# Optimization experiments

Hardware: AMD Instinct MI355X
Metric: run time of the kernel (lower is better)

The kernel has to match this reference:

```python
import jax, jax.numpy as jnp
import numpy as np

IN_F = 4096
OUT_F = 11008
GROUPSIZE = 128
N_GROUPS = IN_F // GROUPSIZE  # 32


def setup_inputs() -> dict:
    key = jax.random.key(0)
    k1, k2, k3, k4 = jax.random.split(key, 4)
    x = jax.random.normal(k1, (4, 2048, IN_F), dtype=jnp.float32)
    # packed 4-bit weights: 8 nibbles per int32 along the input dim
    qweight = jax.random.randint(k2, (IN_F // 8, OUT_F), 0, 2**31 - 1, dtype=jnp.int32)
    # packed 4-bit zero points: 8 nibbles per int32 along the output dim
    qzeros = jax.random.randint(k3, (N_GROUPS, OUT_F // 8), 0, 2**31 - 1, dtype=jnp.int32)
    scales = jax.random.uniform(k4, (N_GROUPS, OUT_F), dtype=jnp.float32,
                                minval=0.001, maxval=0.01)
    g_idx = (jnp.arange(IN_F, dtype=jnp.int32) // GROUPSIZE).astype(jnp.int32)
    return {"x": x, "qweight": qweight, "scales": scales,
            "qzeros": qzeros, "g_idx": g_idx}


def _dequantize(qweight, scales, qzeros, g_idx):
    """GPTQ v2 dequant: W[i, j] = scales[g_idx[i], j] * (q[i, j] - (z[g_idx[i], j] + 1))."""
    shifts = jnp.arange(8, dtype=jnp.int32) * 4  # nibble shift amounts
    # unpack weights along input dim: [in/8, 8, out] -> [in, out]
    q = (qweight[:, None, :] >> shifts[None, :, None]) & 0xF
    q = q.reshape(-1, qweight.shape[1]).astype(scales.dtype)
    # unpack zeros along output dim: [g, out/8, 8] -> [g, out]; +1 per GPTQ v2
    z = ((qzeros[:, :, None] >> shifts[None, None, :]) & 0xF) + 1
    z = z.reshape(qzeros.shape[0], -1).astype(scales.dtype)
    return scales[g_idx] * (q - z[g_idx])  # [in, out]


def reference(x, qweight, scales, qzeros, g_idx):
    W = _dequantize(qweight, scales, qzeros, g_idx)  # [IN_F, OUT_F]
    return jnp.einsum('bsi,io->bso', x, W)
```

## Files before the change

### kernel.cpp

```cpp
#include <hip/hip_runtime.h>
#include <hip/hip_bf16.h>

#define IN_F 4096
#define OUT_F 11008

typedef __bf16 bf16_t;
typedef bf16_t bf16x8 __attribute__((ext_vector_type(8)));
typedef float f32x4 __attribute__((ext_vector_type(4)));
typedef unsigned int u32;

__global__ __launch_bounds__(256) void cvt_x_kernel(const float* __restrict__ x,
                                                    bf16_t* __restrict__ xb) {
    size_t i = ((size_t)blockIdx.x * 256 + threadIdx.x) * 8;
    f32x4 v0 = __builtin_nontemporal_load((const f32x4*)(x + i));
    f32x4 v1 = __builtin_nontemporal_load((const f32x4*)(x + i + 4));
    bf16x8 h;
    h[0]=(bf16_t)v0[0]; h[1]=(bf16_t)v0[1]; h[2]=(bf16_t)v0[2]; h[3]=(bf16_t)v0[3];
    h[4]=(bf16_t)v1[0]; h[5]=(bf16_t)v1[1]; h[6]=(bf16_t)v1[2]; h[7]=(bf16_t)v1[3];
    *(bf16x8*)(xb + i) = h;
}


#define NI (IN_F / 128)

__global__ __launch_bounds__(512, 2) void gemm_dq(const bf16_t* __restrict__ A,
                                                  const int* __restrict__ qweight,
                                                  const float* __restrict__ scales,
                                                  const int* __restrict__ qzeros,
                                                  float* __restrict__ C) {
    __shared__ __align__(16) bf16_t smemA[2 * 2 * 128 * 64];

    const int tid  = threadIdx.x;
    const int lane = tid & 63;
    const int wid  = tid >> 6;
    const int wr   = wid >> 2;
    const int wc   = wid & 3;

    const int bid = blockIdx.x;
    const int swz = (bid & 7) * 172 + (bid >> 3);
    const int bx = swz % 43;
    const int by = swz / 43;
    const int m0 = by * 256;
    const int n0 = bx * 256;

    int lr0, kb0, lr1, kb1;
    {
        int L0 = tid * 16;
        int p0 = L0 ^ (((L0 >> 7) & 7) << 4);
        lr0 = p0 >> 7; kb0 = (p0 & 127) >> 1;
        int L1 = (512 + tid) * 16;
        int p1 = L1 ^ (((L1 >> 7) & 7) << 4);
        lr1 = p1 >> 7; kb1 = (p1 & 127) >> 1;
    }

    const int xm = (lane & 7) << 4;
    const int arow = lane & 15;
    int colk[2];
    #pragma unroll
    for (int ks = 0; ks < 2; ++ks)
        colk[ks] = ((ks * 64) + ((lane >> 4) * 16)) ^ xm;

    const int ncol = n0 + wc * 64 + (lane & 15);
    const int qidx = (lane >> 4) * OUT_F + ncol;
    const int zidx = ncol >> 3;
    const int zsh  = (lane & 7) * 4;

#define STAGE_A(buf, half, koff)                                                           \
    do {                                                                                   \
        const bf16_t* g0_ = A + (size_t)(m0 + (half) * 128 + lr0) * IN_F + (koff) + kb0;   \
        __builtin_amdgcn_global_load_lds(                                                  \
            (const __attribute__((address_space(1))) u32*)g0_,                             \
            (__attribute__((address_space(3))) u32*)((char*)smemA + (buf) * 32768 +        \
                                                     (half) * 16384 + wid * 1024),         \
            16, 0, 0);                                                                     \
        const bf16_t* g1_ = A + (size_t)(m0 + (half) * 128 + lr1) * IN_F + (koff) + kb1;   \
        __builtin_amdgcn_global_load_lds(                                                  \
            (const __attribute__((address_space(1))) u32*)g1_,                             \
            (__attribute__((address_space(3))) u32*)((char*)smemA + (buf) * 32768 +        \
                                                     (half) * 16384 + 8192 + wid * 1024),  \
            16, 0, 0);                                                                     \
    } while (0)

#define RD_A(dst, buf, mbase)                                                              \
    _Pragma("unroll") for (int mm = 0; mm < 4; ++mm)                                       \
    _Pragma("unroll") for (int ks = 0; ks < 2; ++ks)                                       \
        dst[mm * 2 + ks] = *(const bf16x8*)((const char*)smemA + (buf) * 32768 +           \
            wr * 16384 + (((mbase) + mm) * 16 + arow) * 128 + colk[ks]);

#define LOAD_W(rowAbs)                                                                     \
    _Pragma("unroll") for (int nt = 0; nt < 4; ++nt)                                       \
    _Pragma("unroll") for (int ks = 0; ks < 2; ++ks)                                       \
        w[nt * 2 + ks] = ((const u32*)qweight)[qidx + ((rowAbs) + ks * 4) * OUT_F + nt * 16];

#define DEQ(dst, nt0)                                                                      \
    _Pragma("unroll") for (int nn = 0; nn < 2; ++nn)                                       \
    _Pragma("unroll") for (int ks = 0; ks < 2; ++ks) {                                     \
        const u32 wv_ = w[((nt0) + nn) * 2 + ks];                                          \
        const u32 ev_ = wv_ & 0x0F0F0F0Fu;                                                 \
        const u32 od_ = (wv_ >> 4) & 0x0F0F0F0Fu;                                          \
        const float s_ = s0[(nt0) + nn];                                                   \
        const float z_ = nsz0[(nt0) + nn];                                                 \
        bf16x8 h_;                                                                         \
        h_[0] = (bf16_t)fmaf((float)(ev_ & 0xFF), s_, z_);                                 \
        h_[1] = (bf16_t)fmaf((float)(od_ & 0xFF), s_, z_);                                 \
        h_[2] = (bf16_t)fmaf((float)((ev_ >> 8) & 0xFF), s_, z_);                          \
        h_[3] = (bf16_t)fmaf((float)((od_ >> 8) & 0xFF), s_, z_);                          \
        h_[4] = (bf16_t)fmaf((float)((ev_ >> 16) & 0xFF), s_, z_);                         \
        h_[5] = (bf16_t)fmaf((float)((od_ >> 16) & 0xFF), s_, z_);                         \
        h_[6] = (bf16_t)fmaf((float)(ev_ >> 24), s_, z_);                                  \
        h_[7] = (bf16_t)fmaf((float)(od_ >> 24), s_, z_);                                  \
        dst[nn * 2 + ks] = h_;                                                             \
    }

#define MFMA_Q(aArr, bArr, mbase, nbase)                                                   \
    __builtin_amdgcn_s_setprio(1);                                                         \
    _Pragma("unroll") for (int mm = 0; mm < 4; ++mm)                                       \
    _Pragma("unroll") for (int nn = 0; nn < 2; ++nn)                                       \
    _Pragma("unroll") for (int ks = 0; ks < 2; ++ks)                                       \
        acc[(mbase) + mm][(nbase) + nn] = __builtin_amdgcn_mfma_f32_16x16x32_bf16(         \
            aArr[mm * 2 + ks], bArr[nn * 2 + ks], acc[(mbase) + mm][(nbase) + nn],         \
            0, 0, 0);                                                                      \
    __builtin_amdgcn_s_setprio(0);

#define SCHED0() __builtin_amdgcn_sched_barrier(0)
#define BAR() do { SCHED0(); __builtin_amdgcn_s_barrier(); } while (0)
#define VMCNT10() asm volatile("s_waitcnt vmcnt(10)" ::: "memory")
#define VMCNT8()  asm volatile("s_waitcnt vmcnt(8)"  ::: "memory")

    f32x4 acc[8][4];
    #pragma unroll
    for (int m = 0; m < 8; ++m)
        #pragma unroll
        for (int n = 0; n < 4; ++n)
            acc[m][n] = (f32x4)0.0f;

    bf16x8 aR[8], b01[4], b23[4];
    u32   w[8];
    float s0[4], nsz0[4];
    float sraw[4]; u32 zraw[4];

    STAGE_A(0, 0, 0); STAGE_A(0, 1, 0);
    STAGE_A(1, 0, 64);
    LOAD_W(0);
    #pragma unroll
    for (int nt = 0; nt < 4; ++nt) {
        sraw[nt] = scales[ncol + nt * 16];
        zraw[nt] = ((const u32*)qzeros)[zidx + nt * 2];
    }
    #pragma unroll
    for (int nt = 0; nt < 4; ++nt) {
        s0[nt] = sraw[nt];
        nsz0[nt] = -sraw[nt] * (float)(((zraw[nt] >> zsh) & 0xF) + 1);
    }
    BAR();

    for (int i = 0; i < NI; ++i) {
        const int  kc = i * 128;
        const int  kn = kc + 128;
        const int  rw = i * 16;
        const bool nl = (i + 1 < NI);

        RD_A(aR, 0, 0);
        STAGE_A(1, 1, kc + 64);
        DEQ(b01, 0);
        MFMA_Q(aR, b01, 0, 0);
        BAR();
        DEQ(b23, 2);
        MFMA_Q(aR, b23, 0, 2);
        BAR();
        RD_A(aR, 0, 4);
        LOAD_W(rw + 8);
        MFMA_Q(aR, b01, 4, 0);
        BAR();
        if (nl) STAGE_A(0, 0, kn);
        MFMA_Q(aR, b23, 4, 2);
        if (nl) VMCNT10(); else VMCNT8();
        BAR();
        RD_A(aR, 1, 0);
        if (nl) STAGE_A(0, 1, kn);
        DEQ(b01, 0);
        MFMA_Q(aR, b01, 0, 0);
        BAR();
        if (nl) {
            #pragma unroll
            for (int nt = 0; nt < 4; ++nt) {
                sraw[nt] = scales[ncol + (i + 1) * OUT_F + nt * 16];
                zraw[nt] = ((const u32*)qzeros)[zidx + (i + 1) * (OUT_F / 8) + nt * 2];
            }
        }
        DEQ(b23, 2);
        MFMA_Q(aR, b23, 0, 2);
        BAR();
        RD_A(aR, 1, 4);
        if (nl) {
            LOAD_W(rw + 16);
            #pragma unroll
            for (int nt = 0; nt < 4; ++nt) {
                s0[nt] = sraw[nt];
                nsz0[nt] = -sraw[nt] * (float)(((zraw[nt] >> zsh) & 0xF) + 1);
            }
        }
        MFMA_Q(aR, b01, 4, 0);
        BAR();
        if (nl) STAGE_A(1, 0, kn + 64);
        MFMA_Q(aR, b23, 4, 2);
        if (nl) VMCNT10();
        BAR();
    }

    const int cn  = lane & 15;
    const int cr4 = (lane >> 4) * 4;
    #pragma unroll
    for (int m = 0; m < 8; ++m) {
        #pragma unroll
        for (int r = 0; r < 4; ++r) {
            const int grow = m0 + wr * 128 + m * 16 + cr4 + r;
            float* orow = C + (size_t)grow * OUT_F + n0 + wc * 64 + cn;
            #pragma unroll
            for (int n = 0; n < 4; ++n)
                orow[n * 16] = acc[m][n][r];
        }
    }
}

#define BMf 128
#define BNf 128
#define BKf 32
#define LDPF 40

__global__ __launch_bounds__(256, 2) void gptq_gemm_fused(
    const float* __restrict__ x, const int* __restrict__ qweight,
    const float* __restrict__ scales, const int* __restrict__ qzeros,
    float* __restrict__ out)
{
    __shared__ bf16_t As[BMf * LDPF];
    __shared__ bf16_t Bs[BNf * LDPF];
    const int tid = threadIdx.x, lane = tid & 63, wid = tid >> 6;
    const int wr = wid >> 1, wc = wid & 1;
    const int m0 = blockIdx.y * BMf, n0 = blockIdx.x * BNf;
    const int a_row = tid >> 2, a_slot = tid & 3;
    const int b_k8l = tid >> 7, b_n = tid & 127;

    f32x4 acc[4][4];
    #pragma unroll
    for (int i = 0; i < 4; ++i)
        #pragma unroll
        for (int j = 0; j < 4; ++j) acc[i][j] = (f32x4)0.0f;

    for (int kt = 0; kt < IN_F / BKf; ++kt) {
        const int k0 = kt * BKf;
        const int g  = k0 >> 7;
        __syncthreads();
        #pragma unroll
        for (int p = 0; p < 2; ++p) {
            const int row = a_row + p * 64;
            const float* src = x + (size_t)(m0 + row) * IN_F + k0 + a_slot * 8;
            f32x4 v0 = *(const f32x4*)src;
            f32x4 v1 = *(const f32x4*)(src + 4);
            bf16x8 h;
            h[0]=(bf16_t)v0[0]; h[1]=(bf16_t)v0[1]; h[2]=(bf16_t)v0[2]; h[3]=(bf16_t)v0[3];
            h[4]=(bf16_t)v1[0]; h[5]=(bf16_t)v1[1]; h[6]=(bf16_t)v1[2]; h[7]=(bf16_t)v1[3];
            *(bf16x8*)(&As[row * LDPF + a_slot * 8]) = h;
        }
        {
            const int gn = n0 + b_n;
            const float s  = scales[(size_t)g * OUT_F + gn];
            const int   zw = qzeros[(size_t)g * (OUT_F / 8) + (gn >> 3)];
            const float sz = s * (float)(((zw >> ((gn & 7) * 4)) & 0xF) + 1);
            #pragma unroll
            for (int p = 0; p < 2; ++p) {
                const int k8l = b_k8l + p * 2;
                const int w = qweight[(size_t)(k0 / 8 + k8l) * OUT_F + gn];
                bf16x8 h;
                #pragma unroll
                for (int j = 0; j < 8; ++j)
                    h[j] = (bf16_t)fmaf((float)((w >> (4 * j)) & 0xF), s, -sz);
                *(bf16x8*)(&Bs[b_n * LDPF + k8l * 8]) = h;
            }
        }
        __syncthreads();
        bf16x8 af[4], bfr[4];
        #pragma unroll
        for (int m = 0; m < 4; ++m)
            af[m] = *(const bf16x8*)(&As[(wr * 64 + m * 16 + (lane & 15)) * LDPF + (lane >> 4) * 8]);
        #pragma unroll
        for (int n = 0; n < 4; ++n)
            bfr[n] = *(const bf16x8*)(&Bs[(wc * 64 + n * 16 + (lane & 15)) * LDPF + (lane >> 4) * 8]);
        #pragma unroll
        for (int m = 0; m < 4; ++m)
            #pragma unroll
            for (int n = 0; n < 4; ++n)
                acc[m][n] = __builtin_amdgcn_mfma_f32_16x16x32_bf16(af[m], bfr[n], acc[m][n], 0, 0, 0);
    }
    const int cn = lane & 15, cr4 = (lane >> 4) * 4;
    #pragma unroll
    for (int m = 0; m < 4; ++m)
        #pragma unroll
        for (int r = 0; r < 4; ++r) {
            const int grow = m0 + wr * 64 + m * 16 + cr4 + r;
            float* orow = out + (size_t)grow * OUT_F + n0 + wc * 64 + cn;
            #pragma unroll
            for (int n = 0; n < 4; ++n) orow[n * 16] = acc[m][n][r];
        }
}

extern "C" void kernel_launch(void* const* d_in, const int* in_sizes, int n_in,
                              void* d_out, int out_size, void* d_ws, size_t ws_size,
                              hipStream_t stream) {
    const float* x       = (const float*)d_in[0];
    const int*   qweight = (const int*)d_in[1];
    const float* scales  = (const float*)d_in[2];
    const int*   qzeros  = (const int*)d_in[3];
    float* out = (float*)d_out;

    const int M = in_sizes[0] / IN_F;
    const size_t xb_bytes = (size_t)M * IN_F * 2;

    if (ws_size >= xb_bytes && (M % 256) == 0) {
        bf16_t* xb = (bf16_t*)d_ws;
        cvt_x_kernel<<<dim3((M * IN_F) / (256 * 8)), dim3(256), 0, stream>>>(x, xb);
        const int nwg = (OUT_F / 256) * (M / 256);
        gemm_dq<<<dim3(nwg), dim3(512), 0, stream>>>(xb, qweight, scales, qzeros, out);
    } else {
        gptq_gemm_fused<<<dim3(OUT_F / BNf, M / BMf), dim3(256), 0, stream>>>(
            x, qweight, scales, qzeros, out);
    }
}
```

Measured before the change: 1.001 ms.

## Stage packed 4-bit weights through LDS with async global-to-LDS loads

Packed qweight tiles are now loaded cooperatively into a double-buffered shared-memory region with global_load_lds, instead of each wave issuing strided per-lane global loads into registers. Dequantization of a whole k-half is moved to a single point after the corresponding vmcnt wait, and the scale/zero loads are rescheduled earlier. The aim is coalesced 16-byte weight fetches that overlap the MFMA work. The cost is 16 KB of extra LDS, changed wait counts, and dequant bursts that are less interleaved with the MFMAs.

```diff
diff --git a/kernel.cpp b/kernel.cpp
--- a/kernel.cpp
+++ b/kernel.cpp
@@ -23,12 +23,13 @@
 
 #define NI (IN_F / 128)
 
-__global__ __launch_bounds__(512, 2) void gemm_dq(const bf16_t* __restrict__ A,
+__global__ __launch_bounds__(512, 2) void gemm_q4(const bf16_t* __restrict__ A,
                                                   const int* __restrict__ qweight,
                                                   const float* __restrict__ scales,
                                                   const int* __restrict__ qzeros,
                                                   float* __restrict__ C) {
     __shared__ __align__(16) bf16_t smemA[2 * 2 * 128 * 64];
+    __shared__ __align__(16) u32    smemB[2 * 2048];
 
     const int tid  = threadIdx.x;
     const int lane = tid & 63;
@@ -61,9 +62,11 @@
         colk[ks] = ((ks * 64) + ((lane >> 4) * 16)) ^ xm;
 
     const int ncol = n0 + wc * 64 + (lane & 15);
-    const int qidx = (lane >> 4) * OUT_F + ncol;
-    const int zidx = ncol >> 3;
-    const int zsh  = (lane & 7) * 4;
+    const u32* bw = smemB + (wc * 512 + (lane >> 4) * 16 + (lane & 15));
+    const int kwS  = (tid >> 2) & 7;
+    const int colS = (tid >> 5) * 16 + (tid & 3) * 4;
+    const u32* qB = (const u32*)qweight + (size_t)kwS * OUT_F + n0 + colS;
+    const int zsh = (lane & 7) * 4;
 
 #define STAGE_A(buf, half, koff)                                                           \
     do {                                                                                   \
@@ -81,16 +84,22 @@
             16, 0, 0);                                                                     \
     } while (0)
 
+#define STAGE_B(buf, ktrow)                                                                \
+    __builtin_amdgcn_global_load_lds(                                                      \
+        (const __attribute__((address_space(1))) u32*)(qB + (size_t)(ktrow) * OUT_F),      \
+        (__attribute__((address_space(3))) u32*)((char*)smemB + (buf) * 8192 + tid * 16),  \
+        16, 0, 0)
+
 #define RD_A(dst, buf, mbase)                                                              \
     _Pragma("unroll") for (int mm = 0; mm < 4; ++mm)                                       \
     _Pragma("unroll") for (int ks = 0; ks < 2; ++ks)                                       \
         dst[mm * 2 + ks] = *(const bf16x8*)((const char*)smemA + (buf) * 32768 +           \
             wr * 16384 + (((mbase) + mm) * 16 + arow) * 128 + colk[ks]);
 
-#define LOAD_W(rowAbs)                                                                     \
+#define RD_W(buf)                                                                          \
     _Pragma("unroll") for (int nt = 0; nt < 4; ++nt)                                       \
     _Pragma("unroll") for (int ks = 0; ks < 2; ++ks)                                       \
-        w[nt * 2 + ks] = ((const u32*)qweight)[qidx + ((rowAbs) + ks * 4) * OUT_F + nt * 16];
+        w[nt * 2 + ks] = bw[(buf) * 2048 + nt * 128 + ks * 64];
 
 #define DEQ(dst, nt0)                                                                      \
     _Pragma("unroll") for (int nn = 0; nn < 2; ++nn)                                       \
@@ -125,7 +134,8 @@
 #define SCHED0() __builtin_amdgcn_sched_barrier(0)
 #define BAR() do { SCHED0(); __builtin_amdgcn_s_barrier(); } while (0)
 #define VMCNT10() asm volatile("s_waitcnt vmcnt(10)" ::: "memory")
-#define VMCNT8()  asm volatile("s_waitcnt vmcnt(8)"  ::: "memory")
+#define VMCNT2()  asm volatile("s_waitcnt vmcnt(2)"  ::: "memory")
+#define VMCNT0()  asm volatile("s_waitcnt vmcnt(0)"  ::: "memory")
 
     f32x4 acc[8][4];
     #pragma unroll
@@ -140,60 +150,63 @@
     float sraw[4]; u32 zraw[4];
 
     STAGE_A(0, 0, 0); STAGE_A(0, 1, 0);
+    STAGE_B(0, 0);
+    STAGE_B(1, 8);
     STAGE_A(1, 0, 64);
-    LOAD_W(0);
+    VMCNT0();
+    BAR();
     #pragma unroll
     for (int nt = 0; nt < 4; ++nt) {
         sraw[nt] = scales[ncol + nt * 16];
-        zraw[nt] = ((const u32*)qzeros)[zidx + nt * 2];
+        zraw[nt] = ((const u32*)qzeros)[(ncol >> 3) + nt * 2];
     }
     #pragma unroll
     for (int nt = 0; nt < 4; ++nt) {
         s0[nt] = sraw[nt];
         nsz0[nt] = -sraw[nt] * (float)(((zraw[nt] >> zsh) & 0xF) + 1);
     }
+    RD_W(0);
+    DEQ(b01, 0);
+    DEQ(b23, 2);
     BAR();
 
     for (int i = 0; i < NI; ++i) {
         const int  kc = i * 128;
         const int  kn = kc + 128;
-        const int  rw = i * 16;
         const bool nl = (i + 1 < NI);
 
         RD_A(aR, 0, 0);
         STAGE_A(1, 1, kc + 64);
-        DEQ(b01, 0);
+        if (nl) STAGE_B(0, (kn) >> 3);
         MFMA_Q(aR, b01, 0, 0);
         BAR();
-        DEQ(b23, 2);
+        if (nl) {
+            #pragma unroll
+            for (int nt = 0; nt < 4; ++nt) {
+                sraw[nt] = scales[ncol + (i + 1) * OUT_F + nt * 16];
+                zraw[nt] = ((const u32*)qzeros)[(ncol >> 3) + (i + 1) * (OUT_F / 8) + nt * 2];
+            }
+        }
         MFMA_Q(aR, b23, 0, 2);
         BAR();
         RD_A(aR, 0, 4);
-        LOAD_W(rw + 8);
         MFMA_Q(aR, b01, 4, 0);
         BAR();
         if (nl) STAGE_A(0, 0, kn);
         MFMA_Q(aR, b23, 4, 2);
-        if (nl) VMCNT10(); else VMCNT8();
+        if (nl) VMCNT10(); else VMCNT0();
+        RD_W(1);
+        DEQ(b01, 0);
+        DEQ(b23, 2);
         BAR();
         RD_A(aR, 1, 0);
-        if (nl) STAGE_A(0, 1, kn);
-        DEQ(b01, 0);
+        if (nl) { STAGE_A(0, 1, kn); STAGE_B(1, (kn + 64) >> 3); }
         MFMA_Q(aR, b01, 0, 0);
         BAR();
-        if (nl) {
-            #pragma unroll
-            for (int nt = 0; nt < 4; ++nt) {
-                sraw[nt] = scales[ncol + (i + 1) * OUT_F + nt * 16];
-                zraw[nt] = ((const u32*)qzeros)[zidx + (i + 1) * (OUT_F / 8) + nt * 2];
-            }
-        }
-        DEQ(b23, 2);
         MFMA_Q(aR, b23, 0, 2);
         BAR();
         RD_A(aR, 1, 4);
         if (nl) {
-            LOAD_W(rw + 16);
             #pragma unroll
             for (int nt = 0; nt < 4; ++nt) {
                 s0[nt] = sraw[nt];
@@ -204,7 +217,12 @@
         BAR();
         if (nl) STAGE_A(1, 0, kn + 64);
         MFMA_Q(aR, b23, 4, 2);
-        if (nl) VMCNT10();
+        if (nl) VMCNT2(); else VMCNT0();
+        if (nl) {
+            RD_W(0);
+            DEQ(b01, 0);
+            DEQ(b23, 2);
+        }
         BAR();
     }
 
@@ -320,7 +338,7 @@
         bf16_t* xb = (bf16_t*)d_ws;
         cvt_x_kernel<<<dim3((M * IN_F) / (256 * 8)), dim3(256), 0, stream>>>(x, xb);
         const int nwg = (OUT_F / 256) * (M / 256);
-        gemm_dq<<<dim3(nwg), dim3(512), 0, stream>>>(xb, qweight, scales, qzeros, out);
+        gemm_q4<<<dim3(nwg), dim3(512), 0, stream>>>(xb, qweight, scales, qzeros, out);
     } else {
         gptq_gemm_fused<<<dim3(OUT_F / BNf, M / BMf), dim3(256), 0, stream>>>(
             x, qweight, scales, qzeros, out);
```

Measured after the change: 843.8 us. 1.19x faster.
